# Performance work log

Hardware: AMD Instinct MI355X
Metric: run time of the kernel (lower is better)

The kernel has to match this reference:

```python
import jax, jax.numpy as jnp
import numpy as np

N, K, D = 32768, 8192, 64


def setup_inputs() -> dict:
    key = jax.random.key(0)
    k1, k2, k3 = jax.random.split(key, 3)
    z = jax.random.normal(k1, (N, D), dtype=jnp.float32)
    # Riemannian sensitivity weight per sample (positive scalar from decoder VJP norms)
    g_weight = jax.random.uniform(k2, (N,), dtype=jnp.float32)
    # codebook: nn.Embedding(num_embeddings, embedding_dim), weight ~ N(0,1)
    embedding = jax.random.normal(k3, (K, D), dtype=jnp.float32)
    return {"z": z, "g_weight": g_weight, "embedding": embedding}


def reference(z, g_weight, embedding):
    # d(z, e) = ||z||^2 + ||e||^2 - 2 z e^T  -> [N, K]
    z_flat = z.reshape(-1, embedding.shape[1])
    distances = (
        jnp.sum(z_flat * z_flat, axis=1, keepdims=True)
        + jnp.sum(embedding * embedding, axis=1)
        - 2.0 * jnp.matmul(z_flat, embedding.T)
    )
    # Riemannian scaling: d_R = d * G(z)
    riemannian_distances = distances * g_weight[:, None]
    return jnp.argmin(riemannian_distances, axis=1)
```

## Files before the change

kernel.cpp:

```cpp
#include <hip/hip_runtime.h>
#include <hip/hip_fp16.h>
#include <cfloat>
#include <climits>


typedef short  s16x8  __attribute__((ext_vector_type(8)));
typedef float  f32x16 __attribute__((ext_vector_type(16)));

static constexpr int N_ = 32768;
static constexpr int K_ = 8192;
static constexpr int D_ = 64;
static constexpr int NTILES = K_ / 32;
static constexpr int REC_SLOTS = 576;
static constexpr size_t REC_BYTES = (size_t)NTILES * REC_SLOTS * 16;
static constexpr float FLAG_MARGIN = 0.001953125f;
static constexpr float RESID_SCALE = 1024.0f;
static constexpr float RESID_INV   = 0.0009765625f;

struct alignas(16) Part3 { float b1, b2; int i1, pad; };

__device__ __forceinline__ short f2h_s(float x) {
    __half h = __float2half(x);
    return (short)__half_as_short(h);
}

__global__ void rq_prep(const float* __restrict__ emb, s16x8* __restrict__ recs)
{
    __shared__ double sp[32][8];
    const int tile = blockIdx.x;
    const int t = threadIdx.x;
    const int c = t >> 3, q = t & 7;
    const int f = q >> 1, h = q & 1;
    const float* src = emb + (size_t)(tile * 32 + c) * D_ + q * 8;
    float4 a = ((const float4*)src)[0];
    float4 b = ((const float4*)src)[1];
    float e[8] = {a.x, a.y, a.z, a.w, b.x, b.y, b.z, b.w};
    s16x8 u1, u2;
    double s = 0.0;
    #pragma unroll
    for (int j = 0; j < 8; ++j) {
        __half h1 = __float2half(e[j]);
        float r = e[j] - __half2float(h1);
        u1[j] = (short)__half_as_short(h1);
        u2[j] = f2h_s(r * RESID_SCALE);
        s = fma((double)e[j], (double)e[j], s);
    }
    const size_t rb = (size_t)tile * REC_SLOTS;
    recs[rb + f * 64 + h * 32 + c] = u1;
    recs[rb + 320 + f * 64 + h * 32 + c] = u2;
    sp[c][q] = s;
    __syncthreads();
    if (t < 32) {
        double se = 0.0;
        #pragma unroll
        for (int j = 0; j < 8; ++j) se += sp[t][j];
        se *= 0.5;
        float sf = (float)se;
        __half sh = __float2half(sf);
        float  sr = sf - __half2float(sh);
        s16x8 v;
        #pragma unroll
        for (int j = 0; j < 8; ++j) v[j] = 0;
        v[0] = (short)__half_as_short(sh);
        v[1] = f2h_s(sr);
        recs[rb + 256 + t] = v;
    } else if (t < 64) {
        s16x8 v;
        #pragma unroll
        for (int j = 0; j < 8; ++j) v[j] = 0;
        recs[rb + 256 + t] = v;
    }
}

__global__ __launch_bounds__(256)
void rq_main(const float* __restrict__ z,
             const s16x8* __restrict__ recs,
             Part3* __restrict__ parts,
             int tpb )
{
    __shared__ s16x8 lbuf[2][REC_SLOTS];
    const int tid  = threadIdx.x;
    const int wave = tid >> 6, lane = tid & 63;
    const int col  = lane & 31, h = lane >> 5;
    const int slice = blockIdx.y;
    const int tile0 = slice * tpb;
    const int rowbase = blockIdx.x * 128 + wave * 32;
    const int zrow = rowbase + col;

    s16x8 zn1[4], zn2[4];
    #pragma unroll
    for (int f = 0; f < 4; ++f) {
        const float* src = z + (size_t)zrow * D_ + f * 16 + h * 8;
        float4 a = ((const float4*)src)[0];
        float4 b = ((const float4*)src)[1];
        float e[8] = {a.x, a.y, a.z, a.w, b.x, b.y, b.z, b.w};
        #pragma unroll
        for (int j = 0; j < 8; ++j) {
            float zn = -e[j];
            __half h1 = __float2half(zn);
            zn1[f][j] = (short)__half_as_short(h1);
            zn2[f][j] = f2h_s((zn - __half2float(h1)) * RESID_SCALE);
        }
    }
    s16x8 bse;
    #pragma unroll
    for (int j = 0; j < 8; ++j) bse[j] = 0;
    if (h == 0) { bse[0] = (short)0x3C00; bse[1] = (short)0x3C00; }

    f32x16 zacc;
    #pragma unroll
    for (int r = 0; r < 16; ++r) zacc[r] = 0.0f;

    {
        const size_t gb = (size_t)tile0 * REC_SLOTS;
        lbuf[0][tid]       = recs[gb + tid];
        lbuf[0][256 + tid] = recs[gb + 256 + tid];
        if (tid < 64) lbuf[0][512 + tid] = recs[gb + 512 + tid];
    }
    __syncthreads();

    float b1e = FLT_MAX, b2e = FLT_MAX, b1o = FLT_MAX, b2o = FLT_MAX;
    int   i1e = INT_MAX, i1o = INT_MAX;

    for (int t = 0; t < tpb; ++t) {
        const int cb = t & 1, nb = cb ^ 1;
        const bool pf = (t + 1 < tpb);
        s16x8 r0, r1, r2;
        if (pf) {
            const size_t gb = (size_t)(tile0 + t + 1) * REC_SLOTS;
            r0 = recs[gb + tid];
            r1 = recs[gb + 256 + tid];
            if (tid < 64) r2 = recs[gb + 512 + tid];
        }

        s16x8 ea[4], e2a[4], sea;
        #pragma unroll
        for (int f = 0; f < 4; ++f) ea[f]  = lbuf[cb][f * 64 + lane];
        sea = lbuf[cb][256 + lane];
        #pragma unroll
        for (int f = 0; f < 4; ++f) e2a[f] = lbuf[cb][320 + f * 64 + lane];

        f32x16 acc, acc2;
        acc  = __builtin_amdgcn_mfma_f32_32x32x16_f16(sea,    bse,    zacc, 0, 0, 0);
        acc2 = __builtin_amdgcn_mfma_f32_32x32x16_f16(e2a[0], zn1[0], zacc, 0, 0, 0);
        acc  = __builtin_amdgcn_mfma_f32_32x32x16_f16(ea[0],  zn1[0], acc,  0, 0, 0);
        acc2 = __builtin_amdgcn_mfma_f32_32x32x16_f16(e2a[1], zn1[1], acc2, 0, 0, 0);
        acc  = __builtin_amdgcn_mfma_f32_32x32x16_f16(ea[1],  zn1[1], acc,  0, 0, 0);
        acc2 = __builtin_amdgcn_mfma_f32_32x32x16_f16(e2a[2], zn1[2], acc2, 0, 0, 0);
        acc  = __builtin_amdgcn_mfma_f32_32x32x16_f16(ea[2],  zn1[2], acc,  0, 0, 0);
        acc2 = __builtin_amdgcn_mfma_f32_32x32x16_f16(e2a[3], zn1[3], acc2, 0, 0, 0);
        acc  = __builtin_amdgcn_mfma_f32_32x32x16_f16(ea[3],  zn1[3], acc,  0, 0, 0);
        acc2 = __builtin_amdgcn_mfma_f32_32x32x16_f16(ea[0],  zn2[0], acc2, 0, 0, 0);
        acc2 = __builtin_amdgcn_mfma_f32_32x32x16_f16(ea[1],  zn2[1], acc2, 0, 0, 0);
        acc2 = __builtin_amdgcn_mfma_f32_32x32x16_f16(ea[2],  zn2[2], acc2, 0, 0, 0);
        acc2 = __builtin_amdgcn_mfma_f32_32x32x16_f16(ea[3],  zn2[3], acc2, 0, 0, 0);

        const int tb32 = (tile0 + t) * 32;
        #pragma unroll
        for (int r = 0; r < 16; r += 2) {
            float v = fmaf(acc2[r], RESID_INV, acc[r]);
            int cru = tb32 + ((r & 3) + 8 * (r >> 2));
            b2e = fminf(b2e, fmaxf(v, b1e));
            bool lt = v < b1e;
            i1e = lt ? cru : i1e;
            b1e = fminf(b1e, v);
        }
        #pragma unroll
        for (int r = 1; r < 16; r += 2) {
            float v = fmaf(acc2[r], RESID_INV, acc[r]);
            int cru = tb32 + ((r & 3) + 8 * (r >> 2));
            b2o = fminf(b2o, fmaxf(v, b1o));
            bool lt = v < b1o;
            i1o = lt ? cru : i1o;
            b1o = fminf(b1o, v);
        }

        if (pf) {
            lbuf[nb][tid]       = r0;
            lbuf[nb][256 + tid] = r1;
            if (tid < 64) lbuf[nb][512 + tid] = r2;
        }
        __syncthreads();
    }

    float b1, b2; int i1;
    b2 = fminf(fminf(b2e, b2o), fmaxf(b1e, b1o));
    if (b1o < b1e) { b1 = b1o; i1 = i1o; } else { b1 = b1e; i1 = i1e; }
    i1 += 4 * h;

    float ob1 = __shfl_xor(b1, 32);
    float ob2 = __shfl_xor(b2, 32);
    int   oi1 = __shfl_xor(i1, 32);
    float nb2 = fminf(fminf(b2, ob2), fmaxf(b1, ob1));
    if (ob1 < b1) { b1 = ob1; i1 = oi1; }
    b2 = nb2;
    if (lane < 32) {
        Part3 p; p.b1 = b1; p.b2 = b2; p.i1 = i1; p.pad = 0;
        parts[(size_t)slice * N_ + (rowbase + lane)] = p;
    }
}

__global__ void rq_merge(const Part3* __restrict__ parts,
                         const float* __restrict__ g,
                         int* __restrict__ out,
                         int* __restrict__ counter,
                         int* __restrict__ list,
                         int nsl, int maxf)
{
    int row = blockIdx.x * 256 + threadIdx.x;
    Part3 p = parts[row];
    float b1 = p.b1, b2 = p.b2; int i1 = p.i1;
    for (int s = 1; s < nsl; ++s) {
        Part3 q = parts[(size_t)s * N_ + row];
        float m2 = fminf(fminf(b2, q.b2), fmaxf(b1, q.b1));
        if (q.b1 < b1) { b1 = q.b1; i1 = q.i1; }
        b2 = m2;
    }
    if (g[row] == 0.0f) { out[row] = 0; return; }
    out[row] = i1;
    if (b2 - b1 < FLAG_MARGIN) {
        int idx = atomicAdd(counter, 1);
        if (idx < maxf) list[idx] = row;
    }
}

__global__ __launch_bounds__(256)
void rq_cleanup_part(const float* __restrict__ z,
                     const float* __restrict__ emb,
                     const int* __restrict__ counter,
                     const int* __restrict__ list,
                     double* __restrict__ vparts,
                     int* __restrict__ iparts,
                     int maxf)
{
    int cnt = *counter; if (cnt > maxf) cnt = maxf;
    const int jobs = cnt * 8;
    const int wid  = (blockIdx.x * 256 + threadIdx.x) >> 6;
    const int lane = threadIdx.x & 63;
    const int nw   = gridDim.x * 4;

    for (int j = wid; j < jobs; j += nw) {
        const int row = list[j >> 3];
        const int sl  = j & 7;
        float zr[64];
        {
            const float4* zp = reinterpret_cast<const float4*>(z + (size_t)row * D_);
            #pragma unroll
            for (int q = 0; q < 16; ++q) {
                float4 v = zp[q];
                zr[4*q] = v.x; zr[4*q+1] = v.y; zr[4*q+2] = v.z; zr[4*q+3] = v.w;
            }
        }
        double bv = DBL_MAX; int bi = INT_MAX;
        for (int i = 0; i < 16; ++i) {
            const int c = sl * 1024 + i * 64 + lane;
            const float4* ep = reinterpret_cast<const float4*>(emb + (size_t)c * D_);
            double sd0 = 0, sd1 = 0, sq0 = 0, sq1 = 0;
            #pragma unroll
            for (int q = 0; q < 16; ++q) {
                float4 ev = ep[q];
                sd0 = fma((double)ev.x, (double)zr[4*q+0], sd0);
                sq0 = fma((double)ev.x, (double)ev.x, sq0);
                sd1 = fma((double)ev.y, (double)zr[4*q+1], sd1);
                sq1 = fma((double)ev.y, (double)ev.y, sq1);
                sd0 = fma((double)ev.z, (double)zr[4*q+2], sd0);
                sq0 = fma((double)ev.z, (double)ev.z, sq0);
                sd1 = fma((double)ev.w, (double)zr[4*q+3], sd1);
                sq1 = fma((double)ev.w, (double)ev.w, sq1);
            }
            double v = 0.5 * (sq0 + sq1) - (sd0 + sd1);
            if (v < bv) { bv = v; bi = c; }
        }
        #pragma unroll
        for (int m = 1; m < 64; m <<= 1) {
            double ov = __shfl_xor(bv, m);
            int    oi = __shfl_xor(bi, m);
            if (ov < bv || (ov == bv && oi < bi)) { bv = ov; bi = oi; }
        }
        if (lane == 0) { vparts[j] = bv; iparts[j] = bi; }
    }
}

__global__ void rq_cleanup_fin(const int* __restrict__ counter,
                               const int* __restrict__ list,
                               const double* __restrict__ vparts,
                               const int* __restrict__ iparts,
                               int* __restrict__ out, int maxf)
{
    int cnt = *counter; if (cnt > maxf) cnt = maxf;
    int j = blockIdx.x * 256 + threadIdx.x;
    if (j >= cnt) return;
    double bv = vparts[j * 8]; int bi = iparts[j * 8];
    #pragma unroll
    for (int s = 1; s < 8; ++s) {
        double v = vparts[j * 8 + s]; int i = iparts[j * 8 + s];
        if (v < bv || (v == bv && i < bi)) { bv = v; bi = i; }
    }
    out[list[j]] = bi;
}

__global__ __launch_bounds__(256, 4)
void rq_fallback(const float* __restrict__ z,
                 const float* __restrict__ emb,
                 const float* __restrict__ g,
                 int* __restrict__ out)
{
    __shared__ float  lds_e[64][64];
    __shared__ double lds_se[64];
    const int tid = threadIdx.x;
    const int row = blockIdx.x * 256 + tid;
    float zr[64];
    {
        const float4* zp = reinterpret_cast<const float4*>(z + (size_t)row * D_);
        #pragma unroll
        for (int j = 0; j < 16; ++j) {
            float4 v = zp[j];
            zr[4*j] = v.x; zr[4*j+1] = v.y; zr[4*j+2] = v.z; zr[4*j+3] = v.w;
        }
    }
    float best32 = FLT_MAX; double bestv = DBL_MAX; int bestidx = 0;
    for (int t = 0; t < K_; t += 64) {
        __syncthreads();
        {
            const float4* src = reinterpret_cast<const float4*>(emb + (size_t)t * D_);
            float4* dst = reinterpret_cast<float4*>(&lds_e[0][0]);
            #pragma unroll
            for (int j = 0; j < 4; ++j) dst[tid + j * 256] = src[tid + j * 256];
        }
        if (tid < 64) {
            const float* er = emb + (size_t)(t + tid) * D_;
            double s = 0;
            for (int d = 0; d < 64; ++d) s = fma((double)er[d], (double)er[d], s);
            lds_se[tid] = 0.5 * s;
        }
        __syncthreads();
        float cv0 = FLT_MAX, cv1 = FLT_MAX, cv2 = FLT_MAX;
        int ck0 = 0, ck1 = 0, ck2 = 0;
        for (int kk = 0; kk < 64; ++kk) {
            const float4* ep = reinterpret_cast<const float4*>(&lds_e[kk][0]);
            float a0 = 0, a1 = 0, a2 = 0, a3 = 0;
            #pragma unroll
            for (int j = 0; j < 16; ++j) {
                float4 e4 = ep[j];
                a0 = fmaf(zr[4*j], e4.x, a0);   a1 = fmaf(zr[4*j+1], e4.y, a1);
                a2 = fmaf(zr[4*j+2], e4.z, a2); a3 = fmaf(zr[4*j+3], e4.w, a3);
            }
            float val = (float)lds_se[kk] - ((a0 + a1) + (a2 + a3));
            if (val < best32 + 0.0625f) {
                cv2 = cv1; ck2 = ck1; cv1 = cv0; ck1 = ck0;
                cv0 = val; ck0 = kk;
                best32 = fminf(best32, val);
            }
        }
        const float thr = best32 + 0.0625f;
        #pragma unroll
        for (int r = 0; r < 3; ++r) {
            float cv = (r == 0) ? cv2 : (r == 1) ? cv1 : cv0;
            int   ck = (r == 0) ? ck2 : (r == 1) ? ck1 : ck0;
            if (cv < thr) {
                const float4* ep = reinterpret_cast<const float4*>(&lds_e[ck][0]);
                double s0 = 0, s1 = 0, s2 = 0, s3 = 0;
                #pragma unroll
                for (int j = 0; j < 16; ++j) {
                    float4 e4 = ep[j];
                    s0 = fma((double)zr[4*j],   (double)e4.x, s0);
                    s1 = fma((double)zr[4*j+1], (double)e4.y, s1);
                    s2 = fma((double)zr[4*j+2], (double)e4.z, s2);
                    s3 = fma((double)zr[4*j+3], (double)e4.w, s3);
                }
                double vd = lds_se[ck] - ((s0 + s1) + (s2 + s3));
                int kidx = t + ck;
                if (vd < bestv) { bestv = vd; bestidx = kidx; }
                else if (vd == bestv && kidx < bestidx) bestidx = kidx;
            }
        }
    }
    out[row] = (g[row] == 0.0f) ? 0 : bestidx;
}

extern "C" void kernel_launch(void* const* d_in, const int* in_sizes, int n_in,
                              void* d_out, int out_size, void* d_ws, size_t ws_size,
                              hipStream_t stream)
{
    const float* z   = (const float*)d_in[0];
    const float* g   = (const float*)d_in[1];
    const float* emb = (const float*)d_in[2];
    int* out = (int*)d_out;

    auto need = [&](int s, int mf) {
        return REC_BYTES + (size_t)s * N_ * sizeof(Part3) + 64
             + (size_t)mf * 4 + (size_t)mf * 8 * 8 + (size_t)mf * 8 * 4;
    };
    int nsl = 0, maxf = 0;
    const int nsls[4]  = {8, 4, 2, 1};
    const int maxfs[2] = {16384, 2048};
    for (int a = 0; a < 4 && !nsl; ++a)
        for (int b = 0; b < 2; ++b)
            if (need(nsls[a], maxfs[b]) <= ws_size) { nsl = nsls[a]; maxf = maxfs[b]; break; }

    if (!nsl) {
        rq_fallback<<<N_ / 256, 256, 0, stream>>>(z, emb, g, out);
        return;
    }

    char* w = (char*)d_ws;
    s16x8*  recs    = (s16x8*)w;                              w += REC_BYTES;
    Part3*  parts   = (Part3*)w;                              w += (size_t)nsl * N_ * sizeof(Part3);
    int*    counter = (int*)w;                                w += 64;
    int*    list    = (int*)w;                                w += (size_t)maxf * 4;
    double* vparts  = (double*)w;                             w += (size_t)maxf * 8 * 8;
    int*    iparts  = (int*)w;

    rq_prep<<<NTILES, 256, 0, stream>>>(emb, recs);
    hipMemsetAsync(counter, 0, sizeof(int), stream);
    rq_main<<<dim3(N_ / 128, nsl), 256, 0, stream>>>(z, recs, parts, NTILES / nsl);
    rq_merge<<<N_ / 256, 256, 0, stream>>>(parts, g, out, counter, list, nsl, maxf);
    rq_cleanup_part<<<1024, 256, 0, stream>>>(z, emb, counter, list, vparts, iparts, maxf);
    rq_cleanup_fin<<<128, 256, 0, stream>>>(counter, list, vparts, iparts, out, maxf);
}
```

Baseline: 170.6 us.

## Process two row groups per wave and load codebook directly from global memory

Each wave now handles 64 z rows (two 32-row MFMA groups) instead of 32, so every codebook tile fragment it loads is used by twice as many MFMAs, and the shared-memory bias MFMA result is computed once per tile. The LDS double buffer and per-tile __syncthreads are removed; waves read codebook records straight from global memory (cached in L2/L1). The grid is halved in the row dimension. This trades more registers and fewer blocks for lower sync and LDS overhead, and global load latency is no longer hidden by explicit prefetch.

```diff
diff --git a/kernel.cpp b/kernel.cpp
--- a/kernel.cpp
+++ b/kernel.cpp
@@ -23,6 +23,8 @@
     __half h = __float2half(x);
     return (short)__half_as_short(h);
 }
+
+#define MFMA16(A, B, C) __builtin_amdgcn_mfma_f32_32x32x16_f16((A), (B), (C), 0, 0, 0)
 
 __global__ void rq_prep(const float* __restrict__ emb, s16x8* __restrict__ recs)
 {
@@ -78,28 +80,30 @@
              Part3* __restrict__ parts,
              int tpb )
 {
-    __shared__ s16x8 lbuf[2][REC_SLOTS];
     const int tid  = threadIdx.x;
     const int wave = tid >> 6, lane = tid & 63;
     const int col  = lane & 31, h = lane >> 5;
     const int slice = blockIdx.y;
     const int tile0 = slice * tpb;
-    const int rowbase = blockIdx.x * 128 + wave * 32;
-    const int zrow = rowbase + col;
-
-    s16x8 zn1[4], zn2[4];
-    #pragma unroll
-    for (int f = 0; f < 4; ++f) {
-        const float* src = z + (size_t)zrow * D_ + f * 16 + h * 8;
-        float4 a = ((const float4*)src)[0];
-        float4 b = ((const float4*)src)[1];
-        float e[8] = {a.x, a.y, a.z, a.w, b.x, b.y, b.z, b.w};
-        #pragma unroll
-        for (int j = 0; j < 8; ++j) {
-            float zn = -e[j];
-            __half h1 = __float2half(zn);
-            zn1[f][j] = (short)__half_as_short(h1);
-            zn2[f][j] = f2h_s((zn - __half2float(h1)) * RESID_SCALE);
+    const int rowbase = blockIdx.x * 256 + wave * 64;
+
+    s16x8 zn1[2][4], zn2[2][4];
+    #pragma unroll
+    for (int g = 0; g < 2; ++g) {
+        const int zrow = rowbase + 32 * g + col;
+        #pragma unroll
+        for (int f = 0; f < 4; ++f) {
+            const float* src = z + (size_t)zrow * D_ + f * 16 + h * 8;
+            float4 a = ((const float4*)src)[0];
+            float4 b = ((const float4*)src)[1];
+            float e[8] = {a.x, a.y, a.z, a.w, b.x, b.y, b.z, b.w};
+            #pragma unroll
+            for (int j = 0; j < 8; ++j) {
+                float zn = -e[j];
+                __half h1 = __float2half(zn);
+                zn1[g][f][j] = (short)__half_as_short(h1);
+                zn2[g][f][j] = f2h_s((zn - __half2float(h1)) * RESID_SCALE);
+            }
         }
     }
     s16x8 bse;
@@ -111,92 +115,76 @@
     #pragma unroll
     for (int r = 0; r < 16; ++r) zacc[r] = 0.0f;
 
-    {
-        const size_t gb = (size_t)tile0 * REC_SLOTS;
-        lbuf[0][tid]       = recs[gb + tid];
-        lbuf[0][256 + tid] = recs[gb + 256 + tid];
-        if (tid < 64) lbuf[0][512 + tid] = recs[gb + 512 + tid];
-    }
-    __syncthreads();
-
-    float b1e = FLT_MAX, b2e = FLT_MAX, b1o = FLT_MAX, b2o = FLT_MAX;
-    int   i1e = INT_MAX, i1o = INT_MAX;
+    float b1e[2] = {FLT_MAX, FLT_MAX}, b2e[2] = {FLT_MAX, FLT_MAX};
+    float b1o[2] = {FLT_MAX, FLT_MAX}, b2o[2] = {FLT_MAX, FLT_MAX};
+    int   i1e[2] = {INT_MAX, INT_MAX}, i1o[2] = {INT_MAX, INT_MAX};
 
     for (int t = 0; t < tpb; ++t) {
-        const int cb = t & 1, nb = cb ^ 1;
-        const bool pf = (t + 1 < tpb);
-        s16x8 r0, r1, r2;
-        if (pf) {
-            const size_t gb = (size_t)(tile0 + t + 1) * REC_SLOTS;
-            r0 = recs[gb + tid];
-            r1 = recs[gb + 256 + tid];
-            if (tid < 64) r2 = recs[gb + 512 + tid];
-        }
-
+        const s16x8* gp = recs + (size_t)(tile0 + t) * REC_SLOTS;
         s16x8 ea[4], e2a[4], sea;
         #pragma unroll
-        for (int f = 0; f < 4; ++f) ea[f]  = lbuf[cb][f * 64 + lane];
-        sea = lbuf[cb][256 + lane];
-        #pragma unroll
-        for (int f = 0; f < 4; ++f) e2a[f] = lbuf[cb][320 + f * 64 + lane];
-
-        f32x16 acc, acc2;
-        acc  = __builtin_amdgcn_mfma_f32_32x32x16_f16(sea,    bse,    zacc, 0, 0, 0);
-        acc2 = __builtin_amdgcn_mfma_f32_32x32x16_f16(e2a[0], zn1[0], zacc, 0, 0, 0);
-        acc  = __builtin_amdgcn_mfma_f32_32x32x16_f16(ea[0],  zn1[0], acc,  0, 0, 0);
-        acc2 = __builtin_amdgcn_mfma_f32_32x32x16_f16(e2a[1], zn1[1], acc2, 0, 0, 0);
-        acc  = __builtin_amdgcn_mfma_f32_32x32x16_f16(ea[1],  zn1[1], acc,  0, 0, 0);
-        acc2 = __builtin_amdgcn_mfma_f32_32x32x16_f16(e2a[2], zn1[2], acc2, 0, 0, 0);
-        acc  = __builtin_amdgcn_mfma_f32_32x32x16_f16(ea[2],  zn1[2], acc,  0, 0, 0);
-        acc2 = __builtin_amdgcn_mfma_f32_32x32x16_f16(e2a[3], zn1[3], acc2, 0, 0, 0);
-        acc  = __builtin_amdgcn_mfma_f32_32x32x16_f16(ea[3],  zn1[3], acc,  0, 0, 0);
-        acc2 = __builtin_amdgcn_mfma_f32_32x32x16_f16(ea[0],  zn2[0], acc2, 0, 0, 0);
-        acc2 = __builtin_amdgcn_mfma_f32_32x32x16_f16(ea[1],  zn2[1], acc2, 0, 0, 0);
-        acc2 = __builtin_amdgcn_mfma_f32_32x32x16_f16(ea[2],  zn2[2], acc2, 0, 0, 0);
-        acc2 = __builtin_amdgcn_mfma_f32_32x32x16_f16(ea[3],  zn2[3], acc2, 0, 0, 0);
+        for (int f = 0; f < 4; ++f) ea[f]  = gp[f * 64 + lane];
+        sea = gp[256 + lane];
+        #pragma unroll
+        for (int f = 0; f < 4; ++f) e2a[f] = gp[320 + f * 64 + lane];
+
+        f32x16 accSE = MFMA16(sea, bse, zacc);
 
         const int tb32 = (tile0 + t) * 32;
         #pragma unroll
-        for (int r = 0; r < 16; r += 2) {
-            float v = fmaf(acc2[r], RESID_INV, acc[r]);
-            int cru = tb32 + ((r & 3) + 8 * (r >> 2));
-            b2e = fminf(b2e, fmaxf(v, b1e));
-            bool lt = v < b1e;
-            i1e = lt ? cru : i1e;
-            b1e = fminf(b1e, v);
-        }
-        #pragma unroll
-        for (int r = 1; r < 16; r += 2) {
-            float v = fmaf(acc2[r], RESID_INV, acc[r]);
-            int cru = tb32 + ((r & 3) + 8 * (r >> 2));
-            b2o = fminf(b2o, fmaxf(v, b1o));
-            bool lt = v < b1o;
-            i1o = lt ? cru : i1o;
-            b1o = fminf(b1o, v);
-        }
-
-        if (pf) {
-            lbuf[nb][tid]       = r0;
-            lbuf[nb][256 + tid] = r1;
-            if (tid < 64) lbuf[nb][512 + tid] = r2;
-        }
-        __syncthreads();
-    }
-
-    float b1, b2; int i1;
-    b2 = fminf(fminf(b2e, b2o), fmaxf(b1e, b1o));
-    if (b1o < b1e) { b1 = b1o; i1 = i1o; } else { b1 = b1e; i1 = i1e; }
-    i1 += 4 * h;
-
-    float ob1 = __shfl_xor(b1, 32);
-    float ob2 = __shfl_xor(b2, 32);
-    int   oi1 = __shfl_xor(i1, 32);
-    float nb2 = fminf(fminf(b2, ob2), fmaxf(b1, ob1));
-    if (ob1 < b1) { b1 = ob1; i1 = oi1; }
-    b2 = nb2;
-    if (lane < 32) {
-        Part3 p; p.b1 = b1; p.b2 = b2; p.i1 = i1; p.pad = 0;
-        parts[(size_t)slice * N_ + (rowbase + lane)] = p;
+        for (int g = 0; g < 2; ++g) {
+            f32x16 acc, acc2;
+            acc  = MFMA16(ea[0],  zn1[g][0], accSE);
+            acc2 = MFMA16(e2a[0], zn1[g][0], zacc);
+            acc  = MFMA16(ea[1],  zn1[g][1], acc);
+            acc2 = MFMA16(e2a[1], zn1[g][1], acc2);
+            acc  = MFMA16(ea[2],  zn1[g][2], acc);
+            acc2 = MFMA16(e2a[2], zn1[g][2], acc2);
+            acc  = MFMA16(ea[3],  zn1[g][3], acc);
+            acc2 = MFMA16(e2a[3], zn1[g][3], acc2);
+            acc2 = MFMA16(ea[0],  zn2[g][0], acc2);
+            acc2 = MFMA16(ea[1],  zn2[g][1], acc2);
+            acc2 = MFMA16(ea[2],  zn2[g][2], acc2);
+            acc2 = MFMA16(ea[3],  zn2[g][3], acc2);
+
+            #pragma unroll
+            for (int r = 0; r < 16; r += 2) {
+                float v = fmaf(acc2[r], RESID_INV, acc[r]);
+                int cru = tb32 + ((r & 3) + 8 * (r >> 2));
+                b2e[g] = fminf(b2e[g], fmaxf(v, b1e[g]));
+                bool lt = v < b1e[g];
+                i1e[g] = lt ? cru : i1e[g];
+                b1e[g] = fminf(b1e[g], v);
+            }
+            #pragma unroll
+            for (int r = 1; r < 16; r += 2) {
+                float v = fmaf(acc2[r], RESID_INV, acc[r]);
+                int cru = tb32 + ((r & 3) + 8 * (r >> 2));
+                b2o[g] = fminf(b2o[g], fmaxf(v, b1o[g]));
+                bool lt = v < b1o[g];
+                i1o[g] = lt ? cru : i1o[g];
+                b1o[g] = fminf(b1o[g], v);
+            }
+        }
+    }
+
+    #pragma unroll
+    for (int g = 0; g < 2; ++g) {
+        float b1, b2; int i1;
+        b2 = fminf(fminf(b2e[g], b2o[g]), fmaxf(b1e[g], b1o[g]));
+        if (b1o[g] < b1e[g]) { b1 = b1o[g]; i1 = i1o[g]; } else { b1 = b1e[g]; i1 = i1e[g]; }
+        i1 += 4 * h;
+
+        float ob1 = __shfl_xor(b1, 32);
+        float ob2 = __shfl_xor(b2, 32);
+        int   oi1 = __shfl_xor(i1, 32);
+        float nb2 = fminf(fminf(b2, ob2), fmaxf(b1, ob1));
+        if (ob1 < b1) { b1 = ob1; i1 = oi1; }
+        b2 = nb2;
+        if (lane < 32) {
+            Part3 p; p.b1 = b1; p.b2 = b2; p.i1 = i1; p.pad = 0;
+            parts[(size_t)slice * N_ + (rowbase + 32 * g + lane)] = p;
+        }
     }
 }
 
@@ -413,7 +401,7 @@
 
     rq_prep<<<NTILES, 256, 0, stream>>>(emb, recs);
     hipMemsetAsync(counter, 0, sizeof(int), stream);
-    rq_main<<<dim3(N_ / 128, nsl), 256, 0, stream>>>(z, recs, parts, NTILES / nsl);
+    rq_main<<<dim3(N_ / 256, nsl), 256, 0, stream>>>(z, recs, parts, NTILES / nsl);
     rq_merge<<<N_ / 256, 256, 0, stream>>>(parts, g, out, counter, list, nsl, maxf);
     rq_cleanup_part<<<1024, 256, 0, stream>>>(z, emb, counter, list, vparts, iparts, maxf);
     rq_cleanup_fin<<<128, 256, 0, stream>>>(counter, list, vparts, iparts, out, maxf);
```

After: 169.9 us. Within noise of the previous version (-0.4%).
